# Performance work log

Measured on AMD Instinct MI355X. Metric: run time of the kernel, lower is better.

The kernel has to match this reference:

```python
import jax, jax.numpy as jnp
import numpy as np

B, N1, N2, D, H = 32, 512, 256, 256, 8
HD = D // H  # head dim = 32


def setup_inputs() -> dict:
    key = jax.random.key(0)
    ks = jax.random.split(key, 12)
    s = 0.05
    return {
        "x1": jax.random.normal(ks[0], (B, N1, D), jnp.float32),
        "x2": jax.random.normal(ks[1], (B, N2, D), jnp.float32),
        "r_w1": jax.random.normal(ks[2], (D, 2 * D), jnp.float32) * s,
        "r_b1": jnp.zeros((D,), jnp.float32),
        "ln_g": jnp.ones((D,), jnp.float32),
        "ln_b": jnp.zeros((D,), jnp.float32),
        "r_w2": jax.random.normal(ks[3], (4, D), jnp.float32) * s,
        "r_b2": jnp.zeros((4,), jnp.float32),
        "lf_w": jax.random.normal(ks[4], (D, D), jnp.float32) * s,
        "lf_b": jnp.zeros((D,), jnp.float32),
        "af2_w": jax.random.normal(ks[5], (D, D), jnp.float32) * s,
        "af2_b": jnp.zeros((D,), jnp.float32),
        "af3_w": jax.random.normal(ks[6], (N1, D), jnp.float32) * s,  # Linear(dim, num_pathway)
        "af3_b": jnp.zeros((N1,), jnp.float32),
        "attn_in_w": jax.random.normal(ks[7], (3 * D, D), jnp.float32) * s,
        "attn_in_b": jnp.zeros((3 * D,), jnp.float32),
        "attn_out_w": jax.random.normal(ks[8], (D, D), jnp.float32) * s,
        "attn_out_b": jnp.zeros((D,), jnp.float32),
    }


def _layernorm(x, g, b, eps=1e-5):
    mu = x.mean(-1, keepdims=True)
    var = ((x - mu) ** 2).mean(-1, keepdims=True)
    return (x - mu) * jax.lax.rsqrt(var + eps) * g + b


def reference(x1, x2, r_w1, r_b1, ln_g, ln_b, r_w2, r_b2,
              lf_w, lf_b, af2_w, af2_b, af3_w, af3_b,
              attn_in_w, attn_in_b, attn_out_w, attn_out_b):
    b, n1, d = x1.shape
    n2 = x2.shape[1]

    # ---- RoutingNetwork: mean-pool both modalities, small MLP, softmax ----
    m = jnp.concatenate([x1.mean(1), x2.mean(1)], axis=-1)        # [b, 2d]
    h = jax.nn.gelu(_layernorm(m @ r_w1.T + r_b1, ln_g, ln_b), approximate=False)
    logits = h @ r_w2.T + r_b2                                     # [b, 4]
    w = jax.nn.softmax(logits, axis=-1)                            # [b, 4]

    z = jnp.concatenate([x1, x2], axis=1)                          # [b, n1+n2, d]

    # ---- Expert 0: LinearFusion (dropout off at eval) ----
    lf = jax.nn.elu(z @ lf_w.T + lf_b)
    g0, i0 = lf[:, :n1, :], lf[:, n1:, :]

    # ---- Expert 1: AddFusion, n1 >= n2 branch (n2 == dim required) ----
    a1 = jax.nn.elu(x1 @ af2_w.T + af2_b)                          # [b, n1, d]
    a2 = jax.nn.elu(jnp.einsum('bnd,pn->bdp', x2, af3_w) + af3_b)  # [b, d, n1]
    a2 = a2.transpose(0, 2, 1)                                     # [b, n1, d]
    x_out = a1 + a2
    g1, i1 = x_out, x_out[:, :n2, :]

    # ---- Expert 2: AttentionFusion (MHA, 8 heads, self-attn over concat) ----
    qkv = z @ attn_in_w.T + attn_in_b                              # [b, S, 3d]
    q, k, v = jnp.split(qkv, 3, axis=-1)
    S = n1 + n2
    q = q.reshape(b, S, H, HD)
    k = k.reshape(b, S, H, HD)
    v = v.reshape(b, S, H, HD)
    scores = jnp.einsum('bqhd,bkhd->bhqk', q, k) / np.sqrt(HD)
    attn = jax.nn.softmax(scores, axis=-1)
    o = jnp.einsum('bhqk,bkhd->bqhd', attn, v).reshape(b, S, d)
    o = o @ attn_out_w.T + attn_out_b
    g2, i2 = o[:, :n1, :], o[:, n1:, :]

    # ---- Expert 3: IdentityFusion ----
    g3, i3 = x1, x2

    # ---- Soft-routing weighted combine ----
    gene_all = jnp.stack([g0, g1, g2, g3], axis=1)                 # [b, 4, n1, d]
    img_all = jnp.stack([i0, i1, i2, i3], axis=1)                  # [b, 4, n2, d]
    we = w[:, :, None, None]
    gene = (gene_all * we).sum(axis=1)
    img = (img_all * we).sum(axis=1)
    return gene, img
```

## Files before the change

kernel.cpp:

```cpp
#include <hip/hip_runtime.h>
#include <hip/hip_bf16.h>
#include <math.h>

#define B_ 32
#define N1_ 512
#define N2_ 256
#define D_ 256
#define S_ 768
#define IMG_OFF 4194304
#define QSCALE_ (0.17677669529663689f * 1.4426950408889634f)

typedef __attribute__((ext_vector_type(8))) short bf16x8;
typedef __attribute__((ext_vector_type(4))) float f32x4;
#define MFMA16(a, b, c) __builtin_amdgcn_mfma_f32_16x16x32_bf16(a, b, c, 0, 0, 0)

__device__ __forceinline__ ushort f2b(float f) {
  __hip_bfloat16 h = __float2bfloat16(f);
  return __builtin_bit_cast(ushort, h);
}
__device__ __forceinline__ uint pk2(float a, float b) {
  return (uint)f2b(a) | ((uint)f2b(b) << 16);
}
__device__ __forceinline__ float eluf(float v) { return v > 0.f ? v : expm1f(v); }

__global__ __launch_bounds__(256) void k_prep(const float* __restrict__ x1,
                                              const float* __restrict__ x2,
                                              const float* __restrict__ lf_w,
                                              const float* __restrict__ af2_w,
                                              const float* __restrict__ af3_w,
                                              const float* __restrict__ attn_in_w,
                                              const float* __restrict__ attn_out_w,
                                              ushort* __restrict__ zb,
                                              ushort* __restrict__ wb,
                                              float* __restrict__ mp) {
  int t = threadIdx.x;
  if (blockIdx.x >= 256) {
    int g = (blockIdx.x - 256)*256 + t;
    int e0 = g*4;
    const float* src; int loc; float sc = 1.f;
    if (e0 < 65536)       { src = lf_w;       loc = e0; }
    else if (e0 < 131072) { src = af2_w;      loc = e0 - 65536; }
    else if (e0 < 262144) { src = af3_w;      loc = e0 - 131072; }
    else if (e0 < 458752) { src = attn_in_w;  loc = e0 - 262144; if (loc < 65536) sc = QSCALE_; }
    else                  { src = attn_out_w; loc = e0 - 458752; }
    float4 v = *(const float4*)(src + loc);
    *(ushort4*)(wb + e0) = make_ushort4(f2b(v.x*sc), f2b(v.y*sc), f2b(v.z*sc), f2b(v.w*sc));
    return;
  }
  int b = blockIdx.x >> 3, s = blockIdx.x & 7;
  int c = t & 63;
  int rg = t >> 6;
  __shared__ float red[4][260];
  float4 s1 = {0.f, 0.f, 0.f, 0.f};
  for (int i = 0; i < 16; ++i) {
    int r = s*64 + rg*16 + i;
    float4 v = *(const float4*)(x1 + ((size_t)(b*N1_) + r)*D_ + c*4);
    s1.x += v.x; s1.y += v.y; s1.z += v.z; s1.w += v.w;
    uint2 pk; pk.x = pk2(v.x, v.y); pk.y = pk2(v.z, v.w);
    *(uint2*)(zb + (size_t)b*196608 + (size_t)r*256 + c*4) = pk;
  }
  red[rg][c*4+0] = s1.x; red[rg][c*4+1] = s1.y; red[rg][c*4+2] = s1.z; red[rg][c*4+3] = s1.w;
  __syncthreads();
  {
    float v = red[0][t] + red[1][t] + red[2][t] + red[3][t];
    mp[(size_t)(b*8+s)*512 + t] = v * (1.0f/512.0f);
  }
  __syncthreads();
  float4 s2 = {0.f, 0.f, 0.f, 0.f};
  for (int i = 0; i < 8; ++i) {
    int r = s*32 + rg*8 + i;
    float4 v = *(const float4*)(x2 + ((size_t)(b*N2_) + r)*D_ + c*4);
    s2.x += v.x; s2.y += v.y; s2.z += v.z; s2.w += v.w;
    uint2 pk; pk.x = pk2(v.x, v.y); pk.y = pk2(v.z, v.w);
    *(uint2*)(zb + (size_t)b*196608 + (size_t)(512 + r)*256 + c*4) = pk;
  }
  red[rg][c*4+0] = s2.x; red[rg][c*4+1] = s2.y; red[rg][c*4+2] = s2.z; red[rg][c*4+3] = s2.w;
  __syncthreads();
  {
    float v = red[0][t] + red[1][t] + red[2][t] + red[3][t];
    mp[(size_t)(b*8+s)*512 + 256 + t] = v * (1.0f/256.0f);
  }
}

__global__ __launch_bounds__(256) void k_head(const float* __restrict__ mp, const float* __restrict__ r_w1,
                       const float* __restrict__ r_b1, const float* __restrict__ ln_g,
                       const float* __restrict__ ln_b, const float* __restrict__ r_w2,
                       const float* __restrict__ r_b2, float* __restrict__ wout) {
  int b = blockIdx.x;
  int j = threadIdx.x;
  __shared__ __align__(16) float ms[512];
  __shared__ float red[256];
  float a0 = 0.f, a1 = 0.f;
  for (int s = 0; s < 8; ++s) {
    a0 += mp[(size_t)(b*8+s)*512 + j];
    a1 += mp[(size_t)(b*8+s)*512 + 256 + j];
  }
  ms[j] = a0; ms[j+256] = a1;
  __syncthreads();
  float4 accv = {0.f, 0.f, 0.f, 0.f};
  const float4* wrow4 = (const float4*)(r_w1 + (size_t)j*512);
  const float4* ms4 = (const float4*)ms;
  for (int k = 0; k < 128; ++k) {
    float4 w = wrow4[k], m = ms4[k];
    accv.x += w.x*m.x; accv.y += w.y*m.y; accv.z += w.z*m.z; accv.w += w.w*m.w;
  }
  float acc = r_b1[j] + (accv.x + accv.y) + (accv.z + accv.w);
  red[j] = acc; __syncthreads();
  for (int off=128; off>0; off>>=1){ if (j<off) red[j]+=red[j+off]; __syncthreads(); }
  float mu = red[0] * (1.f/256.f); __syncthreads();
  float cd = acc - mu;
  red[j] = cd*cd; __syncthreads();
  for (int off=128; off>0; off>>=1){ if (j<off) red[j]+=red[j+off]; __syncthreads(); }
  float var = red[0]*(1.f/256.f); __syncthreads();
  float xn = cd * rsqrtf(var + 1e-5f) * ln_g[j] + ln_b[j];
  float h = 0.5f*xn*(1.f+erff(xn*0.70710678118654752f));
  float lg[4];
  for (int e=0;e<4;++e){
    red[j] = h * r_w2[e*256 + j]; __syncthreads();
    for (int off=128; off>0; off>>=1){ if (j<off) red[j]+=red[j+off]; __syncthreads(); }
    lg[e] = red[0] + r_b2[e]; __syncthreads();
  }
  if (j==0){
    float mx = fmaxf(fmaxf(lg[0],lg[1]),fmaxf(lg[2],lg[3]));
    float e0=expf(lg[0]-mx),e1=expf(lg[1]-mx),e2=expf(lg[2]-mx),e3=expf(lg[3]-mx);
    float s=e0+e1+e2+e3;
    wout[b*4+0]=e0/s; wout[b*4+1]=e1/s; wout[b*4+2]=e2/s; wout[b*4+3]=e3/s;
  }
}

__global__ __launch_bounds__(256) void k_qkv(const ushort* __restrict__ zb, const ushort* __restrict__ wb,
                      const float* __restrict__ bias,
                      ushort* __restrict__ qo, ushort* __restrict__ kh,
                      ushort* __restrict__ vt) {
  int ct = blockIdx.x, nt = blockIdx.y, b = blockIdx.z;
  int tid = threadIdx.x;
  int lane = tid & 63, wid = tid >> 6;
  int wm = wid >> 1, wn = wid & 1;
  int l15 = lane & 15, quad = lane >> 4;
  __shared__ __align__(16) ushort As[128][72];
  __shared__ __align__(16) ushort Ws[128][72];
  f32x4 acc[4][4] = {};
  int n0 = nt*128, c0 = ct*128;
  int sr = tid >> 1, sc = (tid & 1) * 32;
  const ushort* arow = zb + (size_t)b*196608 + (size_t)(n0+sr)*256;
  const ushort* wrow = wb + 262144 + (size_t)(c0+sr)*256;
  for (int k0 = 0; k0 < 256; k0 += 64) {
    #pragma unroll
    for (int i = 0; i < 4; ++i) {
      *(uint4*)&As[sr][sc + 8*i] = *(const uint4*)(arow + k0 + sc + 8*i);
      *(uint4*)&Ws[sr][sc + 8*i] = *(const uint4*)(wrow + k0 + sc + 8*i);
    }
    __syncthreads();
    #pragma unroll
    for (int kc = 0; kc < 2; ++kc) {
      bf16x8 af[4], bfr[4];
      #pragma unroll
      for (int im = 0; im < 4; ++im) af[im] = *(bf16x8*)&As[wm*64 + im*16 + l15][kc*32 + quad*8];
      #pragma unroll
      for (int in = 0; in < 4; ++in) bfr[in] = *(bf16x8*)&Ws[wn*64 + in*16 + l15][kc*32 + quad*8];
      #pragma unroll
      for (int im = 0; im < 4; ++im)
        #pragma unroll
        for (int in = 0; in < 4; ++in)
          acc[im][in] = MFMA16(af[im], bfr[in], acc[im][in]);
    }
    __syncthreads();
  }
  if (ct < 2) {
    #pragma unroll
    for (int im = 0; im < 4; ++im)
      #pragma unroll
      for (int reg = 0; reg < 4; ++reg) {
        int n = n0 + wm*64 + im*16 + quad*4 + reg;
        #pragma unroll
        for (int in = 0; in < 4; ++in) {
          int c = c0 + wn*64 + in*16 + l15;
          qo[((size_t)(b*S_)+n)*256 + c] = f2b(acc[im][in][reg] + bias[c]*QSCALE_);
        }
      }
  } else if (ct < 4) {
    #pragma unroll
    for (int im = 0; im < 4; ++im)
      #pragma unroll
      for (int reg = 0; reg < 4; ++reg) {
        int n = n0 + wm*64 + im*16 + quad*4 + reg;
        #pragma unroll
        for (int in = 0; in < 4; ++in) {
          int c = c0 + wn*64 + in*16 + l15;
          int kc2 = c - 256; int h = kc2 >> 5, d = kc2 & 31;
          kh[(((size_t)(b*8+h))*S_ + n)*32 + d] = f2b(acc[im][in][reg] + bias[c]);
        }
      }
  } else {
    #pragma unroll
    for (int im = 0; im < 4; ++im) {
      int nb = n0 + wm*64 + im*16 + quad*4;
      #pragma unroll
      for (int in = 0; in < 4; ++in) {
        int c = c0 + wn*64 + in*16 + l15;
        float bs = bias[c];
        int vcol = c - 512; int h = vcol >> 5, d = vcol & 31;
        uint2 pk;
        pk.x = pk2(acc[im][in][0] + bs, acc[im][in][1] + bs);
        pk.y = pk2(acc[im][in][2] + bs, acc[im][in][3] + bs);
        *(uint2*)&vt[(((size_t)(b*8+h))*32 + d)*S_ + nb] = pk;
      }
    }
  }
}

__global__ __launch_bounds__(256) void k_attn(const ushort* __restrict__ qo,
                                              const ushort* __restrict__ kh,
                                              const ushort* __restrict__ vt,
                                              ushort* __restrict__ obuf) {
  int qhf = blockIdx.x, h = blockIdx.y, b = blockIdx.z;
  int tid = threadIdx.x;
  int lane = tid & 63, w = tid >> 6;
  int l15 = lane & 15, quad = lane >> 4;
  __shared__ __align__(16) ushort Ks[64][40];
  __shared__ __align__(16) ushort Vts[32][72];
  __shared__ __align__(16) ushort Ps[4][16][72];

  int qbase = qhf*384 + w*96;
  bf16x8 bq[6];
  #pragma unroll
  for (int u = 0; u < 6; ++u)
    bq[u] = *(const bf16x8*)(qo + ((size_t)(b*S_) + qbase + u*16 + l15)*256 + h*32 + quad*8);

  f32x4 ao[6][2] = {};
  float lacc[6] = {};

  int skr = tid >> 2, skc = (tid & 3) * 8;
  int svd = tid >> 3, svn = (tid & 7) * 8;
  const ushort* khb = kh + ((size_t)(b*8+h))*S_*32;
  const ushort* vtb = vt + ((size_t)(b*8+h))*32*S_;

  for (int kt = 0; kt < 12; ++kt) {
    __syncthreads();
    *(uint4*)&Ks[skr][skc] = *(const uint4*)(khb + (size_t)(kt*64 + skr)*32 + skc);
    *(uint4*)&Vts[svd][svn] = *(const uint4*)(vtb + (size_t)svd*S_ + kt*64 + svn);
    __syncthreads();

    bf16x8 ak[4];
    #pragma unroll
    for (int t = 0; t < 4; ++t) ak[t] = *(bf16x8*)&Ks[t*16 + l15][quad*8];
    bf16x8 av[2][2];
    #pragma unroll
    for (int im = 0; im < 2; ++im)
      #pragma unroll
      for (int kc = 0; kc < 2; ++kc)
        av[im][kc] = *(bf16x8*)&Vts[im*16 + l15][kc*32 + quad*8];

    #pragma unroll
    for (int u = 0; u < 6; ++u) {
      f32x4 sf[4];
      #pragma unroll
      for (int t = 0; t < 4; ++t) {
        f32x4 z = {0.f, 0.f, 0.f, 0.f};
        sf[t] = MFMA16(ak[t], bq[u], z);
      }
      #pragma unroll
      for (int t = 0; t < 4; ++t) {
        float p0 = __builtin_amdgcn_exp2f(sf[t][0]);
        float p1 = __builtin_amdgcn_exp2f(sf[t][1]);
        float p2 = __builtin_amdgcn_exp2f(sf[t][2]);
        float p3 = __builtin_amdgcn_exp2f(sf[t][3]);
        lacc[u] += (p0 + p1) + (p2 + p3);
        uint2 pk;
        pk.x = pk2(p0, p1);
        pk.y = pk2(p2, p3);
        *(uint2*)&Ps[w][l15][t*16 + quad*4] = pk;
      }
      #pragma unroll
      for (int kc = 0; kc < 2; ++kc) {
        bf16x8 bp = *(bf16x8*)&Ps[w][l15][kc*32 + quad*8];
        ao[u][0] = MFMA16(av[0][kc], bp, ao[u][0]);
        ao[u][1] = MFMA16(av[1][kc], bp, ao[u][1]);
      }
    }
  }
  #pragma unroll
  for (int u = 0; u < 6; ++u) {
    float l = lacc[u];
    l += __shfl_xor(l, 16, 64);
    l += __shfl_xor(l, 32, 64);
    float linv = 1.f / l;
    int n = qbase + u*16 + l15;
    ushort* orow = obuf + ((size_t)(b*S_)+n)*256 + h*32;
    #pragma unroll
    for (int im = 0; im < 2; ++im) {
      uint2 pk;
      pk.x = pk2(ao[u][im][0]*linv, ao[u][im][1]*linv);
      pk.y = pk2(ao[u][im][2]*linv, ao[u][im][3]*linv);
      *(uint2*)(orow + im*16 + quad*4) = pk;
    }
  }
}

__global__ __launch_bounds__(256) void k_out(const ushort* __restrict__ zb, const ushort* __restrict__ wb,
                      const ushort* __restrict__ ob,
                      const float* __restrict__ x1, const float* __restrict__ x2,
                      const float* __restrict__ lf_b, const float* __restrict__ af2_b,
                      const float* __restrict__ af3_b, const float* __restrict__ ao_b,
                      const float* __restrict__ wgt, float* __restrict__ out) {
  int dt = blockIdx.x, nt = blockIdx.y, b = blockIdx.z;
  int tid = threadIdx.x;
  int lane = tid & 63, wid = tid >> 6;
  int wm = wid >> 1, wn = wid & 1;
  int l15 = lane & 15, quad = lane >> 4;
  __shared__ __align__(16) ushort A1[64][72];
  __shared__ __align__(16) ushort A2[64][72];
  __shared__ __align__(16) ushort A3[64][72];
  __shared__ __align__(16) ushort A4[64][72];
  __shared__ __align__(16) ushort W1s[64][72];
  __shared__ __align__(16) ushort W2s[64][72];
  __shared__ __align__(16) ushort W3s[64][72];
  __shared__ __align__(16) ushort W4s[64][72];
  f32x4 a_lf[2][2] = {}, a_a1[2][2] = {}, a_a2[2][2] = {}, a_pj[2][2] = {};
  int n0 = nt*64, d0 = dt*64;
  int xr0 = ((nt < 8) ? nt : (nt - 8)) * 64;
  int sr = tid >> 2, scg = (tid & 3) * 16;

  const ushort* p_a1 = zb + (size_t)b*196608 + (size_t)(n0+sr)*256;
  const ushort* p_a2 = zb + (size_t)b*196608 + (size_t)(xr0+sr)*256;
  const ushort* p_a3 = wb + 131072 + (size_t)(xr0+sr)*256;
  const ushort* p_a4 = ob + ((size_t)(b*S_) + n0 + sr)*256;
  const ushort* p_w1 = wb + (size_t)(d0+sr)*256;
  const ushort* p_w2 = wb + 65536 + (size_t)(d0+sr)*256;
  const ushort* p_w4 = wb + 458752 + (size_t)(d0+sr)*256;

  for (int k0 = 0; k0 < 256; k0 += 64) {
    *(uint4*)&A1[sr][scg]    = *(const uint4*)(p_a1 + k0 + scg);
    *(uint4*)&A1[sr][scg+8]  = *(const uint4*)(p_a1 + k0 + scg + 8);
    *(uint4*)&A2[sr][scg]    = *(const uint4*)(p_a2 + k0 + scg);
    *(uint4*)&A2[sr][scg+8]  = *(const uint4*)(p_a2 + k0 + scg + 8);
    *(uint4*)&A3[sr][scg]    = *(const uint4*)(p_a3 + k0 + scg);
    *(uint4*)&A3[sr][scg+8]  = *(const uint4*)(p_a3 + k0 + scg + 8);
    *(uint4*)&A4[sr][scg]    = *(const uint4*)(p_a4 + k0 + scg);
    *(uint4*)&A4[sr][scg+8]  = *(const uint4*)(p_a4 + k0 + scg + 8);
    *(uint4*)&W1s[sr][scg]   = *(const uint4*)(p_w1 + k0 + scg);
    *(uint4*)&W1s[sr][scg+8] = *(const uint4*)(p_w1 + k0 + scg + 8);
    *(uint4*)&W2s[sr][scg]   = *(const uint4*)(p_w2 + k0 + scg);
    *(uint4*)&W2s[sr][scg+8] = *(const uint4*)(p_w2 + k0 + scg + 8);
    *(uint4*)&W4s[sr][scg]   = *(const uint4*)(p_w4 + k0 + scg);
    *(uint4*)&W4s[sr][scg+8] = *(const uint4*)(p_w4 + k0 + scg + 8);
    {
      const ushort* x2r = zb + (size_t)b*196608 + (size_t)(512 + k0 + sr)*256 + d0 + scg;
      uint4 va = *(const uint4*)x2r;
      uint4 vb = *(const uint4*)(x2r + 8);
      const ushort* ea = (const ushort*)&va;
      const ushort* eb = (const ushort*)&vb;
      #pragma unroll
      for (int i = 0; i < 8; ++i) W3s[scg + i][sr] = ea[i];
      #pragma unroll
      for (int i = 0; i < 8; ++i) W3s[scg + 8 + i][sr] = eb[i];
    }
    __syncthreads();
    #pragma unroll
    for (int kc = 0; kc < 2; ++kc) {
      int ko = kc*32 + quad*8;
      bf16x8 x0, x1r, y0, y1;
      x0 = *(bf16x8*)&A1[wm*32 + l15][ko];  x1r = *(bf16x8*)&A1[wm*32 + 16 + l15][ko];
      y0 = *(bf16x8*)&W1s[wn*32 + l15][ko]; y1  = *(bf16x8*)&W1s[wn*32 + 16 + l15][ko];
      a_lf[0][0] = MFMA16(x0, y0, a_lf[0][0]);  a_lf[0][1] = MFMA16(x0, y1, a_lf[0][1]);
      a_lf[1][0] = MFMA16(x1r, y0, a_lf[1][0]); a_lf[1][1] = MFMA16(x1r, y1, a_lf[1][1]);
      x0 = *(bf16x8*)&A2[wm*32 + l15][ko];  x1r = *(bf16x8*)&A2[wm*32 + 16 + l15][ko];
      y0 = *(bf16x8*)&W2s[wn*32 + l15][ko]; y1  = *(bf16x8*)&W2s[wn*32 + 16 + l15][ko];
      a_a1[0][0] = MFMA16(x0, y0, a_a1[0][0]);  a_a1[0][1] = MFMA16(x0, y1, a_a1[0][1]);
      a_a1[1][0] = MFMA16(x1r, y0, a_a1[1][0]); a_a1[1][1] = MFMA16(x1r, y1, a_a1[1][1]);
      x0 = *(bf16x8*)&A3[wm*32 + l15][ko];  x1r = *(bf16x8*)&A3[wm*32 + 16 + l15][ko];
      y0 = *(bf16x8*)&W3s[wn*32 + l15][ko]; y1  = *(bf16x8*)&W3s[wn*32 + 16 + l15][ko];
      a_a2[0][0] = MFMA16(x0, y0, a_a2[0][0]);  a_a2[0][1] = MFMA16(x0, y1, a_a2[0][1]);
      a_a2[1][0] = MFMA16(x1r, y0, a_a2[1][0]); a_a2[1][1] = MFMA16(x1r, y1, a_a2[1][1]);
      x0 = *(bf16x8*)&A4[wm*32 + l15][ko];  x1r = *(bf16x8*)&A4[wm*32 + 16 + l15][ko];
      y0 = *(bf16x8*)&W4s[wn*32 + l15][ko]; y1  = *(bf16x8*)&W4s[wn*32 + 16 + l15][ko];
      a_pj[0][0] = MFMA16(x0, y0, a_pj[0][0]);  a_pj[0][1] = MFMA16(x0, y1, a_pj[0][1]);
      a_pj[1][0] = MFMA16(x1r, y0, a_pj[1][0]); a_pj[1][1] = MFMA16(x1r, y1, a_pj[1][1]);
    }
    __syncthreads();
  }
  float w0 = wgt[b*4+0], w1v = wgt[b*4+1], w2v = wgt[b*4+2], w3 = wgt[b*4+3];
  #pragma unroll
  for (int im = 0; im < 2; ++im) {
    #pragma unroll
    for (int reg = 0; reg < 4; ++reg) {
      int rl = wm*32 + im*16 + quad*4 + reg;
      int n = n0 + rl;
      int rx = xr0 + rl;
      const float* zr; float* orw;
      if (nt < 8) { zr = x1 + ((size_t)(b*N1_) + n)*D_;      orw = out + ((size_t)(b*N1_) + n)*D_; }
      else { int j2 = n - 512; zr = x2 + ((size_t)(b*N2_) + j2)*D_;
             orw = out + (size_t)IMG_OFF + ((size_t)(b*N2_) + j2)*D_; }
      float b3 = af3_b[rx];
      #pragma unroll
      for (int in = 0; in < 2; ++in) {
        int d = d0 + wn*32 + in*16 + l15;
        float v = w0*eluf(a_lf[im][in][reg] + lf_b[d])
                + w1v*(eluf(a_a1[im][in][reg] + af2_b[d]) + eluf(a_a2[im][in][reg] + b3))
                + w2v*(a_pj[im][in][reg] + ao_b[d])
                + w3*zr[d];
        orw[d] = v;
      }
    }
  }
}

extern "C" void kernel_launch(void* const* d_in, const int* in_sizes, int n_in,
                              void* d_out, int out_size, void* d_ws, size_t ws_size,
                              hipStream_t stream) {
  const float* x1        = (const float*)d_in[0];
  const float* x2        = (const float*)d_in[1];
  const float* r_w1      = (const float*)d_in[2];
  const float* r_b1      = (const float*)d_in[3];
  const float* ln_g      = (const float*)d_in[4];
  const float* ln_b      = (const float*)d_in[5];
  const float* r_w2      = (const float*)d_in[6];
  const float* r_b2      = (const float*)d_in[7];
  const float* lf_b      = (const float*)d_in[9];
  const float* af2_b     = (const float*)d_in[11];
  const float* af3_b     = (const float*)d_in[13];
  const float* attn_in_b = (const float*)d_in[15];
  const float* attn_out_b= (const float*)d_in[17];
  float* out = (float*)d_out;

  float* ws_mp = (float*)d_ws;
  float* ws_w  = ws_mp + 131072;
  ushort* ws_zb = (ushort*)(ws_w + 128);
  ushort* ws_qo = ws_zb + (size_t)B_*S_*256;
  ushort* ws_kh = ws_qo + (size_t)B_*S_*256;
  ushort* ws_vt = ws_kh + (size_t)B_*S_*256;
  ushort* ws_wb = ws_vt + (size_t)B_*S_*256;

  k_prep<<<dim3(768), 256, 0, stream>>>(x1, x2, (const float*)d_in[8], (const float*)d_in[10],
                                        (const float*)d_in[12], (const float*)d_in[14],
                                        (const float*)d_in[16], ws_zb, ws_wb, ws_mp);
  k_head<<<dim3(B_),   256, 0, stream>>>(ws_mp, r_w1, r_b1, ln_g, ln_b, r_w2, r_b2, ws_w);
  k_qkv <<<dim3(6,6,B_), 256, 0, stream>>>(ws_zb, ws_wb, attn_in_b, ws_qo, ws_kh, ws_vt);
  k_attn<<<dim3(2,8,B_), 256, 0, stream>>>(ws_qo, ws_kh, ws_vt, ws_qo);
  k_out <<<dim3(4,12,B_),256, 0, stream>>>(ws_zb, ws_wb, ws_qo, x1, x2,
                                           lf_b, af2_b, af3_b, attn_out_b, ws_w, out);
}
```

Measured before the change: 260.8 us.

## Pre-transpose x2 in prep kernel and shrink k_out K-tile

The prep kernel now also writes a transposed bf16 copy of x2 per batch, staged through shared memory. k_out can then load the af3 operand with plain vector loads instead of a scattered transpose into shared memory inside its K loop. k_out's K tile drops from 64 to 32, halving LDS use to allow more resident blocks at the cost of twice as many barriers. The identity-expert term now reads the bf16 copy of the input instead of fp32 x1/x2, which cuts memory traffic but lowers the precision of that term.

```diff
diff --git a/kernel.cpp b/kernel.cpp
--- a/kernel.cpp
+++ b/kernel.cpp
@@ -20,6 +20,9 @@
 }
 __device__ __forceinline__ uint pk2(float a, float b) {
   return (uint)f2b(a) | ((uint)f2b(b) << 16);
+}
+__device__ __forceinline__ float b2f(ushort u) {
+  return __builtin_bit_cast(float, ((uint)u) << 16);
 }
 __device__ __forceinline__ float eluf(float v) { return v > 0.f ? v : expm1f(v); }
 
@@ -32,6 +35,7 @@
                                               const float* __restrict__ attn_out_w,
                                               ushort* __restrict__ zb,
                                               ushort* __restrict__ wb,
+                                              ushort* __restrict__ x2t,
                                               float* __restrict__ mp) {
   int t = threadIdx.x;
   if (blockIdx.x >= 256) {
@@ -51,6 +55,7 @@
   int c = t & 63;
   int rg = t >> 6;
   __shared__ float red[4][260];
+  __shared__ ushort xt[32][266];
   float4 s1 = {0.f, 0.f, 0.f, 0.f};
   for (int i = 0; i < 16; ++i) {
     int r = s*64 + rg*16 + i;
@@ -68,17 +73,30 @@
   __syncthreads();
   float4 s2 = {0.f, 0.f, 0.f, 0.f};
   for (int i = 0; i < 8; ++i) {
-    int r = s*32 + rg*8 + i;
+    int rl = rg*8 + i;
+    int r = s*32 + rl;
     float4 v = *(const float4*)(x2 + ((size_t)(b*N2_) + r)*D_ + c*4);
     s2.x += v.x; s2.y += v.y; s2.z += v.z; s2.w += v.w;
-    uint2 pk; pk.x = pk2(v.x, v.y); pk.y = pk2(v.z, v.w);
+    ushort b0 = f2b(v.x), b1 = f2b(v.y), b2 = f2b(v.z), b3 = f2b(v.w);
+    uint2 pk; pk.x = (uint)b0 | ((uint)b1 << 16); pk.y = (uint)b2 | ((uint)b3 << 16);
     *(uint2*)(zb + (size_t)b*196608 + (size_t)(512 + r)*256 + c*4) = pk;
+    xt[rl][c*4+0] = b0; xt[rl][c*4+1] = b1; xt[rl][c*4+2] = b2; xt[rl][c*4+3] = b3;
   }
   red[rg][c*4+0] = s2.x; red[rg][c*4+1] = s2.y; red[rg][c*4+2] = s2.z; red[rg][c*4+3] = s2.w;
   __syncthreads();
   {
     float v = red[0][t] + red[1][t] + red[2][t] + red[3][t];
     mp[(size_t)(b*8+s)*512 + 256 + t] = v * (1.0f/256.0f);
+  }
+  ushort* dst = x2t + (size_t)b*65536 + (size_t)t*256 + s*32;
+  #pragma unroll
+  for (int g = 0; g < 4; ++g) {
+    uint4 w;
+    w.x = (uint)xt[g*8+0][t] | ((uint)xt[g*8+1][t] << 16);
+    w.y = (uint)xt[g*8+2][t] | ((uint)xt[g*8+3][t] << 16);
+    w.z = (uint)xt[g*8+4][t] | ((uint)xt[g*8+5][t] << 16);
+    w.w = (uint)xt[g*8+6][t] | ((uint)xt[g*8+7][t] << 16);
+    *(uint4*)(dst + g*8) = w;
   }
 }
 
@@ -298,8 +316,7 @@
 }
 
 __global__ __launch_bounds__(256) void k_out(const ushort* __restrict__ zb, const ushort* __restrict__ wb,
-                      const ushort* __restrict__ ob,
-                      const float* __restrict__ x1, const float* __restrict__ x2,
+                      const ushort* __restrict__ ob, const ushort* __restrict__ x2t,
                       const float* __restrict__ lf_b, const float* __restrict__ af2_b,
                       const float* __restrict__ af3_b, const float* __restrict__ ao_b,
                       const float* __restrict__ wgt, float* __restrict__ out) {
@@ -308,57 +325,40 @@
   int lane = tid & 63, wid = tid >> 6;
   int wm = wid >> 1, wn = wid & 1;
   int l15 = lane & 15, quad = lane >> 4;
-  __shared__ __align__(16) ushort A1[64][72];
-  __shared__ __align__(16) ushort A2[64][72];
-  __shared__ __align__(16) ushort A3[64][72];
-  __shared__ __align__(16) ushort A4[64][72];
-  __shared__ __align__(16) ushort W1s[64][72];
-  __shared__ __align__(16) ushort W2s[64][72];
-  __shared__ __align__(16) ushort W3s[64][72];
-  __shared__ __align__(16) ushort W4s[64][72];
+  __shared__ __align__(16) ushort A1[64][36];
+  __shared__ __align__(16) ushort A2[64][36];
+  __shared__ __align__(16) ushort A3[64][36];
+  __shared__ __align__(16) ushort A4[64][36];
+  __shared__ __align__(16) ushort W1s[64][36];
+  __shared__ __align__(16) ushort W2s[64][36];
+  __shared__ __align__(16) ushort W3s[64][36];
+  __shared__ __align__(16) ushort W4s[64][36];
   f32x4 a_lf[2][2] = {}, a_a1[2][2] = {}, a_a2[2][2] = {}, a_pj[2][2] = {};
   int n0 = nt*64, d0 = dt*64;
   int xr0 = ((nt < 8) ? nt : (nt - 8)) * 64;
-  int sr = tid >> 2, scg = (tid & 3) * 16;
-
-  const ushort* p_a1 = zb + (size_t)b*196608 + (size_t)(n0+sr)*256;
-  const ushort* p_a2 = zb + (size_t)b*196608 + (size_t)(xr0+sr)*256;
-  const ushort* p_a3 = wb + 131072 + (size_t)(xr0+sr)*256;
-  const ushort* p_a4 = ob + ((size_t)(b*S_) + n0 + sr)*256;
-  const ushort* p_w1 = wb + (size_t)(d0+sr)*256;
-  const ushort* p_w2 = wb + 65536 + (size_t)(d0+sr)*256;
-  const ushort* p_w4 = wb + 458752 + (size_t)(d0+sr)*256;
-
-  for (int k0 = 0; k0 < 256; k0 += 64) {
-    *(uint4*)&A1[sr][scg]    = *(const uint4*)(p_a1 + k0 + scg);
-    *(uint4*)&A1[sr][scg+8]  = *(const uint4*)(p_a1 + k0 + scg + 8);
-    *(uint4*)&A2[sr][scg]    = *(const uint4*)(p_a2 + k0 + scg);
-    *(uint4*)&A2[sr][scg+8]  = *(const uint4*)(p_a2 + k0 + scg + 8);
-    *(uint4*)&A3[sr][scg]    = *(const uint4*)(p_a3 + k0 + scg);
-    *(uint4*)&A3[sr][scg+8]  = *(const uint4*)(p_a3 + k0 + scg + 8);
-    *(uint4*)&A4[sr][scg]    = *(const uint4*)(p_a4 + k0 + scg);
-    *(uint4*)&A4[sr][scg+8]  = *(const uint4*)(p_a4 + k0 + scg + 8);
-    *(uint4*)&W1s[sr][scg]   = *(const uint4*)(p_w1 + k0 + scg);
-    *(uint4*)&W1s[sr][scg+8] = *(const uint4*)(p_w1 + k0 + scg + 8);
-    *(uint4*)&W2s[sr][scg]   = *(const uint4*)(p_w2 + k0 + scg);
-    *(uint4*)&W2s[sr][scg+8] = *(const uint4*)(p_w2 + k0 + scg + 8);
-    *(uint4*)&W4s[sr][scg]   = *(const uint4*)(p_w4 + k0 + scg);
-    *(uint4*)&W4s[sr][scg+8] = *(const uint4*)(p_w4 + k0 + scg + 8);
+  int sr = tid >> 2, sc4 = (tid & 3) * 8;
+
+  const ushort* p_a1 = zb + (size_t)b*196608 + (size_t)(n0+sr)*256 + sc4;
+  const ushort* p_a2 = zb + (size_t)b*196608 + (size_t)(xr0+sr)*256 + sc4;
+  const ushort* p_a3 = wb + 131072 + (size_t)(xr0+sr)*256 + sc4;
+  const ushort* p_a4 = ob + ((size_t)(b*S_) + n0 + sr)*256 + sc4;
+  const ushort* p_w1 = wb + (size_t)(d0+sr)*256 + sc4;
+  const ushort* p_w2 = wb + 65536 + (size_t)(d0+sr)*256 + sc4;
+  const ushort* p_w3 = x2t + (size_t)b*65536 + (size_t)(d0+sr)*256 + sc4;
+  const ushort* p_w4 = wb + 458752 + (size_t)(d0+sr)*256 + sc4;
+
+  for (int k0 = 0; k0 < 256; k0 += 32) {
+    *(uint4*)&A1[sr][sc4]  = *(const uint4*)(p_a1 + k0);
+    *(uint4*)&A2[sr][sc4]  = *(const uint4*)(p_a2 + k0);
+    *(uint4*)&A3[sr][sc4]  = *(const uint4*)(p_a3 + k0);
+    *(uint4*)&A4[sr][sc4]  = *(const uint4*)(p_a4 + k0);
+    *(uint4*)&W1s[sr][sc4] = *(const uint4*)(p_w1 + k0);
+    *(uint4*)&W2s[sr][sc4] = *(const uint4*)(p_w2 + k0);
+    *(uint4*)&W3s[sr][sc4] = *(const uint4*)(p_w3 + k0);
+    *(uint4*)&W4s[sr][sc4] = *(const uint4*)(p_w4 + k0);
+    __syncthreads();
     {
-      const ushort* x2r = zb + (size_t)b*196608 + (size_t)(512 + k0 + sr)*256 + d0 + scg;
-      uint4 va = *(const uint4*)x2r;
-      uint4 vb = *(const uint4*)(x2r + 8);
-      const ushort* ea = (const ushort*)&va;
-      const ushort* eb = (const ushort*)&vb;
-      #pragma unroll
-      for (int i = 0; i < 8; ++i) W3s[scg + i][sr] = ea[i];
-      #pragma unroll
-      for (int i = 0; i < 8; ++i) W3s[scg + 8 + i][sr] = eb[i];
-    }
-    __syncthreads();
-    #pragma unroll
-    for (int kc = 0; kc < 2; ++kc) {
-      int ko = kc*32 + quad*8;
+      int ko = quad*8;
       bf16x8 x0, x1r, y0, y1;
       x0 = *(bf16x8*)&A1[wm*32 + l15][ko];  x1r = *(bf16x8*)&A1[wm*32 + 16 + l15][ko];
       y0 = *(bf16x8*)&W1s[wn*32 + l15][ko]; y1  = *(bf16x8*)&W1s[wn*32 + 16 + l15][ko];
@@ -387,10 +387,9 @@
       int rl = wm*32 + im*16 + quad*4 + reg;
       int n = n0 + rl;
       int rx = xr0 + rl;
-      const float* zr; float* orw;
-      if (nt < 8) { zr = x1 + ((size_t)(b*N1_) + n)*D_;      orw = out + ((size_t)(b*N1_) + n)*D_; }
-      else { int j2 = n - 512; zr = x2 + ((size_t)(b*N2_) + j2)*D_;
-             orw = out + (size_t)IMG_OFF + ((size_t)(b*N2_) + j2)*D_; }
+      const ushort* zr = zb + (size_t)b*196608 + (size_t)n*256;
+      float* orw = (nt < 8) ? out + ((size_t)(b*N1_) + n)*D_
+                            : out + (size_t)IMG_OFF + ((size_t)(b*N2_) + (n - 512))*D_;
       float b3 = af3_b[rx];
       #pragma unroll
       for (int in = 0; in < 2; ++in) {
@@ -398,7 +397,7 @@
         float v = w0*eluf(a_lf[im][in][reg] + lf_b[d])
                 + w1v*(eluf(a_a1[im][in][reg] + af2_b[d]) + eluf(a_a2[im][in][reg] + b3))
                 + w2v*(a_pj[im][in][reg] + ao_b[d])
-                + w3*zr[d];
+                + w3*b2f(zr[d]);
         orw[d] = v;
       }
     }
@@ -430,13 +429,14 @@
   ushort* ws_kh = ws_qo + (size_t)B_*S_*256;
   ushort* ws_vt = ws_kh + (size_t)B_*S_*256;
   ushort* ws_wb = ws_vt + (size_t)B_*S_*256;
+  ushort* ws_xt = ws_wb + 524288;
 
   k_prep<<<dim3(768), 256, 0, stream>>>(x1, x2, (const float*)d_in[8], (const float*)d_in[10],
                                         (const float*)d_in[12], (const float*)d_in[14],
-                                        (const float*)d_in[16], ws_zb, ws_wb, ws_mp);
+                                        (const float*)d_in[16], ws_zb, ws_wb, ws_xt, ws_mp);
   k_head<<<dim3(B_),   256, 0, stream>>>(ws_mp, r_w1, r_b1, ln_g, ln_b, r_w2, r_b2, ws_w);
   k_qkv <<<dim3(6,6,B_), 256, 0, stream>>>(ws_zb, ws_wb, attn_in_b, ws_qo, ws_kh, ws_vt);
   k_attn<<<dim3(2,8,B_), 256, 0, stream>>>(ws_qo, ws_kh, ws_vt, ws_qo);
-  k_out <<<dim3(4,12,B_),256, 0, stream>>>(ws_zb, ws_wb, ws_qo, x1, x2,
+  k_out <<<dim3(4,12,B_),256, 0, stream>>>(ws_zb, ws_wb, ws_qo, ws_xt,
                                            lf_b, af2_b, af3_b, attn_out_b, ws_w, out);
 }
```

After: 253.1 us. -3.0%, faster.
